# Performance work log

Hardware: AMD Instinct MI355X
Metric: run time of the kernel (lower is better)

## Reference

```python
import jax, jax.numpy as jnp
import numpy as np

TEMPERATURE = 0.2


def setup_inputs() -> dict:
    key = jax.random.key(0)
    k1, k2 = jax.random.split(key)
    B, D = 4096, 256
    emb_i = jax.random.normal(k1, (B, D), dtype=jnp.float32)
    emb_j = jax.random.normal(k2, (B, D), dtype=jnp.float32)
    return {"emb_i": emb_i, "emb_j": emb_j}


def _nt_xent(emb_i, emb_j, temperature):
    B = emb_i.shape[0]
    # L2-normalize each embedding (F.normalize, dim=1)
    z_i = emb_i / jnp.linalg.norm(emb_i, axis=1, keepdims=True)
    z_j = emb_j / jnp.linalg.norm(emb_j, axis=1, keepdims=True)
    z = jnp.concatenate([z_i, z_j], axis=0)  # [2B, D], unit rows
    # cosine similarity of unit vectors == dot product: single GEMM instead of
    # the O(N^2 D) broadcasted intermediate in the torch source
    sim = z @ z.T  # [2B, 2B]
    # positives: diag(sim, +B) and diag(sim, -B)
    sim_ij = jnp.einsum('bd,bd->b', z_i, z_j)  # == diag(sim, B)
    positives = jnp.concatenate([sim_ij, sim_ij], axis=0)  # [2B]
    exp_sim = jnp.exp(sim / temperature)
    # mask out self-similarity on the main diagonal
    denom = jnp.sum(exp_sim, axis=1) - jnp.diagonal(exp_sim)
    loss_partial = -(positives / temperature - jnp.log(denom))
    return jnp.sum(loss_partial) / (2 * B)


def reference(emb_i, emb_j):
    return _nt_xent(emb_i, emb_j, TEMPERATURE)
```

## Files before the change

kernel.cpp:

```cpp
#include <hip/hip_runtime.h>
#include <hip/hip_bf16.h>

#define D_DIM 256
#define TEMP 0.2f
#define ZSCALE 2.6857913f

typedef __bf16 bf16x8 __attribute__((ext_vector_type(8)));
typedef float f32x4 __attribute__((ext_vector_type(4)));

typedef const __attribute__((address_space(1))) void* gptr_t;
typedef __attribute__((address_space(3))) void* lptr_t;

__global__ __launch_bounds__(256) void nt_normalize(
    const float* __restrict__ ei, const float* __restrict__ ej,
    ushort* __restrict__ z, float* __restrict__ pos, int B) {
  int b = blockIdx.x;
  int d = threadIdx.x;
  float xi = ei[(size_t)b * D_DIM + d];
  float xj = ej[(size_t)b * D_DIM + d];
  float si = xi * xi, sj = xj * xj, sij = xi * xj;
  for (int off = 1; off < 64; off <<= 1) {
    si  += __shfl_xor(si, off);
    sj  += __shfl_xor(sj, off);
    sij += __shfl_xor(sij, off);
  }
  __shared__ float red[3][4];
  int wv = threadIdx.x >> 6, lane = threadIdx.x & 63;
  if (lane == 0) { red[0][wv] = si; red[1][wv] = sj; red[2][wv] = sij; }
  __syncthreads();
  si  = red[0][0] + red[0][1] + red[0][2] + red[0][3];
  sj  = red[1][0] + red[1][1] + red[1][2] + red[1][3];
  sij = red[2][0] + red[2][1] + red[2][2] + red[2][3];
  float ri = rsqrtf(si), rj = rsqrtf(sj);
  __hip_bfloat16 zi = __float2bfloat16(xi * ri * ZSCALE);
  __hip_bfloat16 zj = __float2bfloat16(xj * rj * ZSCALE);
  z[(size_t)b * D_DIM + d]       = *reinterpret_cast<ushort*>(&zi);
  z[(size_t)(B + b) * D_DIM + d] = *reinterpret_cast<ushort*>(&zj);
  if (threadIdx.x == 0) pos[b] = sij * ri * rj;
}

#define BM 128
#define BK 128
#define TGRID 64

__global__ __launch_bounds__(256, 2) void nt_gemm_rowsum(
    const ushort* __restrict__ z, float* __restrict__ partial, int N) {
  int k = blockIdx.x;
  int rt = (int)((2 * TGRID + 1 -
                  sqrtf((float)((2 * TGRID + 1) * (2 * TGRID + 1) - 8 * k))) * 0.5f);
  if (rt > TGRID - 1) rt = TGRID - 1;
  if (rt < 0) rt = 0;
  while (rt > 0 && k < rt * (2 * TGRID - rt + 1) / 2) --rt;
  while (k >= (rt + 1) * (2 * TGRID - rt) / 2) ++rt;
  int ct = rt + (k - rt * (2 * TGRID - rt + 1) / 2);

  __shared__ __align__(16) ushort As[BM * BK];
  __shared__ __align__(16) ushort Bs[BM * BK];
  int t = threadIdx.x;
  int lane = t & 63;
  int wv = t >> 6;
  int wr = wv >> 1, wc = wv & 1;

  f32x4 acc[4][4];
#pragma unroll
  for (int m = 0; m < 4; ++m)
#pragma unroll
    for (int n = 0; n < 4; ++n) acc[m][n] = f32x4{0.f, 0.f, 0.f, 0.f};

  const char* zb = (const char*)z;
  char* asb = (char*)As;
  char* bsb = (char*)Bs;

#pragma unroll
  for (int kt = 0; kt < D_DIM / BK; ++kt) {
#pragma unroll
    for (int p = 0; p < 8; ++p) {
      int chunk = p * 256 + t;
      int row = chunk >> 4;
      int c = chunk & 15;
      int cl = c ^ (row & 7);
      const char* ga = zb + (size_t)(rt * BM + row) * 512 + kt * 256 + cl * 16;
      const char* gb = zb + (size_t)(ct * BM + row) * 512 + kt * 256 + cl * 16;
      __builtin_amdgcn_global_load_lds((gptr_t)ga, (lptr_t)(asb + chunk * 16), 16, 0, 0);
      __builtin_amdgcn_global_load_lds((gptr_t)gb, (lptr_t)(bsb + chunk * 16), 16, 0, 0);
    }
    __syncthreads();
#pragma unroll
    for (int ks = 0; ks < BK / 32; ++ks) {
      bf16x8 af[4], bfr[4];
      int kbyte = ks * 64 + (lane >> 4) * 16;
#pragma unroll
      for (int m = 0; m < 4; ++m) {
        int r = wr * 64 + m * 16 + (lane & 15);
        int addr = ((r << 8) + kbyte) ^ ((r & 7) << 4);
        af[m] = *reinterpret_cast<const bf16x8*>(asb + addr);
      }
#pragma unroll
      for (int n = 0; n < 4; ++n) {
        int r = wc * 64 + n * 16 + (lane & 15);
        int addr = ((r << 8) + kbyte) ^ ((r & 7) << 4);
        bfr[n] = *reinterpret_cast<const bf16x8*>(bsb + addr);
      }
#pragma unroll
      for (int m = 0; m < 4; ++m)
#pragma unroll
        for (int n = 0; n < 4; ++n)
          acc[m][n] = __builtin_amdgcn_mfma_f32_16x16x32_bf16(af[m], bfr[n], acc[m][n], 0, 0, 0);
    }
    __syncthreads();
  }

  bool isdiag = (rt == ct);
  int rbase = rt * BM + wr * 64;
  int cbase = ct * BM + wc * 64 + (lane & 15);
#pragma unroll
  for (int m = 0; m < 4; ++m)
#pragma unroll
    for (int n = 0; n < 4; ++n)
#pragma unroll
      for (int j = 0; j < 4; ++j) {
        int rowg = rbase + m * 16 + (lane >> 4) * 4 + j;
        int colg = cbase + n * 16;
        float e = exp2f(acc[m][n][j]);
        acc[m][n][j] = (isdiag && rowg == colg) ? 0.f : e;
      }
#pragma unroll
  for (int m = 0; m < 4; ++m)
#pragma unroll
    for (int j = 0; j < 4; ++j) {
      float rs = acc[m][0][j] + acc[m][1][j] + acc[m][2][j] + acc[m][3][j];
      rs += __shfl_xor(rs, 1);
      rs += __shfl_xor(rs, 2);
      rs += __shfl_xor(rs, 4);
      rs += __shfl_xor(rs, 8);
      if ((lane & 15) == 0) {
        int rowg = rbase + m * 16 + (lane >> 4) * 4 + j;
        partial[(size_t)(2 * ct + wc) * N + rowg] = rs;
      }
    }
  if (!isdiag) {
#pragma unroll
    for (int n = 0; n < 4; ++n) {
      float cs = 0.f;
#pragma unroll
      for (int m = 0; m < 4; ++m)
#pragma unroll
        for (int j = 0; j < 4; ++j) cs += acc[m][n][j];
      cs += __shfl_xor(cs, 16);
      cs += __shfl_xor(cs, 32);
      if ((lane >> 4) == 0) {
        int colg = cbase + n * 16;
        partial[(size_t)(2 * rt + wr) * N + colg] = cs;
      }
    }
  }
}

__global__ __launch_bounds__(256) void nt_rowfinish(
    const float* __restrict__ partial, const float* __restrict__ pos,
    float* __restrict__ rowfinal, int N, int B) {
  int r = blockIdx.x * blockDim.x + threadIdx.x;
  if (r >= N) return;
  float s = 0.f;
#pragma unroll 8
  for (int p = 0; p < 128; ++p) s += partial[(size_t)p * N + r];
  float pv = pos[r < B ? r : r - B];
  rowfinal[r] = logf(s) - pv * (1.0f / TEMP);
}

__global__ __launch_bounds__(1024) void nt_final(
    const float* __restrict__ rowfinal, float* __restrict__ out, int N) {
  float s = 0.f;
  for (int i = threadIdx.x; i < N; i += 1024) s += rowfinal[i];
  for (int off = 1; off < 64; off <<= 1) s += __shfl_xor(s, off);
  __shared__ float red[16];
  int wv = threadIdx.x >> 6, lane = threadIdx.x & 63;
  if (lane == 0) red[wv] = s;
  __syncthreads();
  if (threadIdx.x == 0) {
    float tot = 0.f;
#pragma unroll
    for (int i = 0; i < 16; ++i) tot += red[i];
    out[0] = tot / (float)N;
  }
}

extern "C" void kernel_launch(void* const* d_in, const int* in_sizes, int n_in,
                              void* d_out, int out_size, void* d_ws, size_t ws_size,
                              hipStream_t stream) {
  const float* ei = (const float*)d_in[0];
  const float* ej = (const float*)d_in[1];
  int B = in_sizes[0] / D_DIM;
  int N = 2 * B;

  char* ws = (char*)d_ws;
  ushort* z      = (ushort*)ws;
  float* partial = (float*)(ws + (size_t)N * D_DIM * 2);
  float* pos     = (float*)(ws + (size_t)N * D_DIM * 2 + (size_t)128 * N * 4);
  float* rowfinal = pos + B;
  float* out = (float*)d_out;

  nt_normalize<<<B, 256, 0, stream>>>(ei, ej, z, pos, B);
  int nblocks = TGRID * (TGRID + 1) / 2;
  nt_gemm_rowsum<<<nblocks, 256, 0, stream>>>(z, partial, N);
  nt_rowfinish<<<(N + 255) / 256, 256, 0, stream>>>(partial, pos, rowfinal, N, B);
  nt_final<<<1, 1024, 0, stream>>>(rowfinal, out, N);
}
```

Measured before the change: 62.82 us.

## Make GEMM-rowsum persistent with register-resident A panel and prefetched B tiles

Replaces one block per triangular tile with a persistent grid of 512 blocks, each walking a contiguous range of upper-triangle tiles. The A row panel (full K=256) is held in registers across tiles that share the same row tile, so it is loaded only when the row changes. The next B panel is issued into LDS before the exp/reduction epilogue so load latency overlaps with epilogue work. Blocks are remapped across XCDs by interleaving. The cost is much higher register pressure (af[8][4] bf16x8) and a 64KB single-buffered LDS tile, which may reduce occupancy.

```diff
diff --git a/kernel.cpp b/kernel.cpp
--- a/kernel.cpp
+++ b/kernel.cpp
@@ -4,6 +4,9 @@
 #define D_DIM 256
 #define TEMP 0.2f
 #define ZSCALE 2.6857913f
+#define TGRID 64
+#define NB 512
+#define NTILES 2080
 
 typedef __bf16 bf16x8 __attribute__((ext_vector_type(8)));
 typedef float f32x4 __attribute__((ext_vector_type(4)));
@@ -39,118 +42,133 @@
   if (threadIdx.x == 0) pos[b] = sij * ri * rj;
 }
 
-#define BM 128
-#define BK 128
-#define TGRID 64
-
 __global__ __launch_bounds__(256, 2) void nt_gemm_rowsum(
     const ushort* __restrict__ z, float* __restrict__ partial, int N) {
-  int k = blockIdx.x;
-  int rt = (int)((2 * TGRID + 1 -
-                  sqrtf((float)((2 * TGRID + 1) * (2 * TGRID + 1) - 8 * k))) * 0.5f);
-  if (rt > TGRID - 1) rt = TGRID - 1;
-  if (rt < 0) rt = 0;
-  while (rt > 0 && k < rt * (2 * TGRID - rt + 1) / 2) --rt;
-  while (k >= (rt + 1) * (2 * TGRID - rt) / 2) ++rt;
-  int ct = rt + (k - rt * (2 * TGRID - rt + 1) / 2);
-
-  __shared__ __align__(16) ushort As[BM * BK];
-  __shared__ __align__(16) ushort Bs[BM * BK];
-  int t = threadIdx.x;
-  int lane = t & 63;
-  int wv = t >> 6;
+  int hw = blockIdx.x;
+  int b = (hw & 7) * (NB / 8) + (hw >> 3);
+  int s = (b * NTILES) / NB;
+  int e = ((b + 1) * NTILES) / NB;
+
+  int rem = s, rt = 0;
+  while (rem >= TGRID - rt) { rem -= TGRID - rt; ++rt; }
+  int ct = rt + rem;
+
+  __shared__ __align__(16) ushort Bs[128 * 256];
+  char* bsb = (char*)Bs;
+  const char* zb = (const char*)z;
+
+  int t = threadIdx.x, lane = t & 63, wv = t >> 6;
   int wr = wv >> 1, wc = wv & 1;
 
-  f32x4 acc[4][4];
-#pragma unroll
-  for (int m = 0; m < 4; ++m)
-#pragma unroll
-    for (int n = 0; n < 4; ++n) acc[m][n] = f32x4{0.f, 0.f, 0.f, 0.f};
-
-  const char* zb = (const char*)z;
-  char* asb = (char*)As;
-  char* bsb = (char*)Bs;
-
-#pragma unroll
-  for (int kt = 0; kt < D_DIM / BK; ++kt) {
-#pragma unroll
-    for (int p = 0; p < 8; ++p) {
+  auto STAGE = [&](int panel) {
+#pragma unroll
+    for (int p = 0; p < 16; ++p) {
       int chunk = p * 256 + t;
-      int row = chunk >> 4;
-      int c = chunk & 15;
+      int row = chunk >> 5;
+      int c = chunk & 31;
       int cl = c ^ (row & 7);
-      const char* ga = zb + (size_t)(rt * BM + row) * 512 + kt * 256 + cl * 16;
-      const char* gb = zb + (size_t)(ct * BM + row) * 512 + kt * 256 + cl * 16;
-      __builtin_amdgcn_global_load_lds((gptr_t)ga, (lptr_t)(asb + chunk * 16), 16, 0, 0);
-      __builtin_amdgcn_global_load_lds((gptr_t)gb, (lptr_t)(bsb + chunk * 16), 16, 0, 0);
-    }
-    __syncthreads();
-#pragma unroll
-    for (int ks = 0; ks < BK / 32; ++ks) {
-      bf16x8 af[4], bfr[4];
-      int kbyte = ks * 64 + (lane >> 4) * 16;
-#pragma unroll
-      for (int m = 0; m < 4; ++m) {
-        int r = wr * 64 + m * 16 + (lane & 15);
-        int addr = ((r << 8) + kbyte) ^ ((r & 7) << 4);
-        af[m] = *reinterpret_cast<const bf16x8*>(asb + addr);
-      }
+      const char* g = zb + (size_t)(panel * 128 + row) * 512 + cl * 16;
+      __builtin_amdgcn_global_load_lds((gptr_t)g, (lptr_t)(bsb + chunk * 16), 16, 0, 0);
+    }
+  };
+
+  bf16x8 af[8][4];
+  int cur_rt = -1;
+  bool staged = false;
+
+  for (int idx = s; idx < e; ++idx) {
+    if (rt != cur_rt) {
+      STAGE(rt);
+      __syncthreads();
+#pragma unroll
+      for (int ks = 0; ks < 8; ++ks)
+#pragma unroll
+        for (int m = 0; m < 4; ++m) {
+          int r = wr * 64 + m * 16 + (lane & 15);
+          int addr = ((r << 9) + ks * 64 + ((lane >> 4) << 4)) ^ ((r & 7) << 4);
+          af[ks][m] = *reinterpret_cast<const bf16x8*>(bsb + addr);
+        }
+      __syncthreads();
+      cur_rt = rt;
+      STAGE(ct);
+      __syncthreads();
+    } else if (!staged) {
+      STAGE(ct);
+      __syncthreads();
+    } else {
+      __syncthreads();
+    }
+
+    f32x4 acc[4][4];
+#pragma unroll
+    for (int m = 0; m < 4; ++m)
+#pragma unroll
+      for (int n = 0; n < 4; ++n) acc[m][n] = f32x4{0.f, 0.f, 0.f, 0.f};
+#pragma unroll
+    for (int ks = 0; ks < 8; ++ks) {
+      bf16x8 bfr[4];
 #pragma unroll
       for (int n = 0; n < 4; ++n) {
         int r = wc * 64 + n * 16 + (lane & 15);
-        int addr = ((r << 8) + kbyte) ^ ((r & 7) << 4);
+        int addr = ((r << 9) + ks * 64 + ((lane >> 4) << 4)) ^ ((r & 7) << 4);
         bfr[n] = *reinterpret_cast<const bf16x8*>(bsb + addr);
       }
 #pragma unroll
       for (int m = 0; m < 4; ++m)
 #pragma unroll
         for (int n = 0; n < 4; ++n)
-          acc[m][n] = __builtin_amdgcn_mfma_f32_16x16x32_bf16(af[m], bfr[n], acc[m][n], 0, 0, 0);
-    }
+          acc[m][n] = __builtin_amdgcn_mfma_f32_16x16x32_bf16(af[ks][m], bfr[n], acc[m][n], 0, 0, 0);
+    }
+    int srt = rt, sct = ct;
     __syncthreads();
-  }
-
-  bool isdiag = (rt == ct);
-  int rbase = rt * BM + wr * 64;
-  int cbase = ct * BM + wc * 64 + (lane & 15);
-#pragma unroll
-  for (int m = 0; m < 4; ++m)
-#pragma unroll
-    for (int n = 0; n < 4; ++n)
+
+    ++ct;
+    if (ct == TGRID) { ++rt; ct = rt; }
+    staged = false;
+    if (idx + 1 < e && rt == cur_rt) { STAGE(ct); staged = true; }
+
+    bool isdiag = (srt == sct);
+    int rbase = srt * 128 + wr * 64;
+    int cbase = sct * 128 + wc * 64 + (lane & 15);
+#pragma unroll
+    for (int m = 0; m < 4; ++m)
+#pragma unroll
+      for (int n = 0; n < 4; ++n)
+#pragma unroll
+        for (int j = 0; j < 4; ++j) {
+          int rowg = rbase + m * 16 + (lane >> 4) * 4 + j;
+          int colg = cbase + n * 16;
+          float ex = exp2f(acc[m][n][j]);
+          acc[m][n][j] = (isdiag && rowg == colg) ? 0.f : ex;
+        }
+#pragma unroll
+    for (int m = 0; m < 4; ++m)
 #pragma unroll
       for (int j = 0; j < 4; ++j) {
-        int rowg = rbase + m * 16 + (lane >> 4) * 4 + j;
-        int colg = cbase + n * 16;
-        float e = exp2f(acc[m][n][j]);
-        acc[m][n][j] = (isdiag && rowg == colg) ? 0.f : e;
+        float rs = acc[m][0][j] + acc[m][1][j] + acc[m][2][j] + acc[m][3][j];
+        rs += __shfl_xor(rs, 1);
+        rs += __shfl_xor(rs, 2);
+        rs += __shfl_xor(rs, 4);
+        rs += __shfl_xor(rs, 8);
+        if ((lane & 15) == 0) {
+          int rowg = rbase + m * 16 + (lane >> 4) * 4 + j;
+          partial[(size_t)(2 * sct + wc) * N + rowg] = rs;
+        }
       }
-#pragma unroll
-  for (int m = 0; m < 4; ++m)
-#pragma unroll
-    for (int j = 0; j < 4; ++j) {
-      float rs = acc[m][0][j] + acc[m][1][j] + acc[m][2][j] + acc[m][3][j];
-      rs += __shfl_xor(rs, 1);
-      rs += __shfl_xor(rs, 2);
-      rs += __shfl_xor(rs, 4);
-      rs += __shfl_xor(rs, 8);
-      if ((lane & 15) == 0) {
-        int rowg = rbase + m * 16 + (lane >> 4) * 4 + j;
-        partial[(size_t)(2 * ct + wc) * N + rowg] = rs;
-      }
-    }
-  if (!isdiag) {
-#pragma unroll
-    for (int n = 0; n < 4; ++n) {
-      float cs = 0.f;
-#pragma unroll
-      for (int m = 0; m < 4; ++m)
-#pragma unroll
-        for (int j = 0; j < 4; ++j) cs += acc[m][n][j];
-      cs += __shfl_xor(cs, 16);
-      cs += __shfl_xor(cs, 32);
-      if ((lane >> 4) == 0) {
-        int colg = cbase + n * 16;
-        partial[(size_t)(2 * rt + wr) * N + colg] = cs;
+    if (!isdiag) {
+#pragma unroll
+      for (int n = 0; n < 4; ++n) {
+        float cs = 0.f;
+#pragma unroll
+        for (int m = 0; m < 4; ++m)
+#pragma unroll
+          for (int j = 0; j < 4; ++j) cs += acc[m][n][j];
+        cs += __shfl_xor(cs, 16);
+        cs += __shfl_xor(cs, 32);
+        if ((lane >> 4) == 0) {
+          int colg = cbase + n * 16;
+          partial[(size_t)(2 * srt + wr) * N + colg] = cs;
+        }
       }
     }
   }
@@ -201,8 +219,7 @@
   float* out = (float*)d_out;
 
   nt_normalize<<<B, 256, 0, stream>>>(ei, ej, z, pos, B);
-  int nblocks = TGRID * (TGRID + 1) / 2;
-  nt_gemm_rowsum<<<nblocks, 256, 0, stream>>>(z, partial, N);
+  nt_gemm_rowsum<<<NB, 256, 0, stream>>>(z, partial, N);
   nt_rowfinish<<<(N + 255) / 256, 256, 0, stream>>>(partial, pos, rowfinal, N, B);
   nt_final<<<1, 1024, 0, stream>>>(rowfinal, out, N);
 }
```

Result: slower. 162.5 us (+158.6%).
